# Optimization experiments

Hardware: AMD Instinct MI355X
Metric: run time of the kernel (lower is better)

Reference implementation:

```python
import jax, jax.numpy as jnp
import numpy as np

B, T, D, H = 2, 2048, 512, 8
HD = D // H  # head_dim = 64


def setup_inputs() -> dict:
    key = jax.random.key(0)
    k1, k2, k3, k4 = jax.random.split(key, 4)
    scale = 1.0 / np.sqrt(D)
    x = jax.random.normal(k1, (B, T, D), dtype=jnp.float32)
    periods = jax.random.randint(k2, (B, H), 0, 64, dtype=jnp.int32)
    w_qkv = jax.random.normal(k3, (3 * D, D), dtype=jnp.float32) * scale
    b_qkv = jnp.zeros((3 * D,), dtype=jnp.float32)
    w_out = jax.random.normal(k4, (D, D), dtype=jnp.float32) * scale
    b_out = jnp.zeros((D,), dtype=jnp.float32)
    return {"x": x, "periods": periods, "w_qkv": w_qkv, "b_qkv": b_qkv,
            "w_out": w_out, "b_out": b_out}


def reference(x, periods, w_qkv, b_qkv, w_out, b_out):
    # qkv projection: (B,T,3D) -> (3,B,H,T,HD)
    qkv = x @ w_qkv.T + b_qkv
    qkv = qkv.reshape(B, T, 3, H, HD).transpose(2, 0, 3, 1, 4)
    q, k, v = qkv[0], qkv[1], qkv[2]

    # periodic-causal mask: valid iff j <= i and (i-j) % p == 0, p = max(period,1)
    i_idx = jnp.arange(T, dtype=jnp.int32)[:, None]   # (T,1)
    j_idx = jnp.arange(T, dtype=jnp.int32)[None, :]   # (1,T)
    diff = i_idx - j_idx                              # (T,T)
    p = jnp.maximum(periods, 1)[:, :, None, None]     # (B,H,1,1)
    valid = (diff >= 0) & ((diff % p) == 0)           # (B,H,T,T)

    scores = jnp.einsum('bhqd,bhkd->bhqk', q, k) / np.sqrt(HD)
    scores = jnp.where(valid, scores, jnp.finfo(scores.dtype).min)
    attn = jax.nn.softmax(scores, axis=-1)

    out = jnp.einsum('bhqk,bhkd->bhqd', attn, v)
    out = out.transpose(0, 2, 1, 3).reshape(B, T, D)
    return out @ w_out.T + b_out
```

## Files before the change

kernel.cpp:

```cpp
#include <hip/hip_runtime.h>
#include <math.h>

#define B_  2
#define T_  2048
#define D_  512
#define H_  8
#define HD_ 64
#define QKVS (3*D_)

typedef __bf16 bf16x8 __attribute__((ext_vector_type(8)));
typedef float  f32x4  __attribute__((ext_vector_type(4)));

__device__ inline unsigned short f2bf(float f) {
  unsigned int u = __float_as_uint(f);
  return (unsigned short)((u + 0x7FFFu + ((u >> 16) & 1u)) >> 16);
}
__device__ inline unsigned int pack2bf(float lo, float hi) {
  return (unsigned int)f2bf(lo) | ((unsigned int)f2bf(hi) << 16);
}

__global__ void cast_all(const float* __restrict__ x,
                         const float* __restrict__ wq,
                         const float* __restrict__ wo,
                         unsigned short* __restrict__ xb,
                         unsigned short* __restrict__ wqb,
                         unsigned short* __restrict__ wob) {
  const int n_x  = (B_ * T_ * D_) / 4;
  const int n_wq = (QKVS * D_) / 4;
  const int n_wo = (D_ * D_) / 4;
  int i = blockIdx.x * blockDim.x + threadIdx.x;
  const float* src; unsigned short* dst; int off;
  if (i < n_x)                    { src = x;  dst = xb;  off = i; }
  else if (i < n_x + n_wq)        { src = wq; dst = wqb; off = i - n_x; }
  else if (i < n_x + n_wq + n_wo) { src = wo; dst = wob; off = i - n_x - n_wq; }
  else return;
  float4 v = ((const float4*)src)[off];
  ushort4 o;
  o.x = f2bf(v.x); o.y = f2bf(v.y); o.z = f2bf(v.z); o.w = f2bf(v.w);
  ((ushort4*)dst)[off] = o;
}

template<int BF16OUT>
__global__ __launch_bounds__(256, 4)
void gemm_nt_64(const unsigned short* __restrict__ A,
                const unsigned short* __restrict__ Bw,
                const float* __restrict__ bias, void* __restrict__ Cv,
                int M, int N, int K) {
  __shared__ short Asd[2][64 * 32];
  __shared__ short Bsd[2][64 * 32];

  const int tid = threadIdx.x;
  const int w   = tid >> 6;
  const int l   = tid & 63;
  const int wr  = w >> 1;
  const int wc  = w & 1;
  const int q   = l >> 4;
  const int ml  = l & 15;
  const int srow = tid >> 2;
  const int kch  = (tid & 3) * 8;

  const int rowbase = blockIdx.y * 64;
  const int colbase = blockIdx.x * 64;

  f32x4 acc[2][2] = {};

  for (int k0 = 0; k0 < K; k0 += 64) {
    __syncthreads();
    #pragma unroll
    for (int pnl = 0; pnl < 2; ++pnl) {
      const int kp = k0 + pnl * 32;
      const unsigned short* ga =
          A + (size_t)(rowbase + srow) * K + kp + kch;
      __builtin_amdgcn_global_load_lds(
          (const __attribute__((address_space(1))) void*)ga,
          (__attribute__((address_space(3))) void*)&Asd[pnl][w * 512],
          16, 0, 0);
      const unsigned short* gb =
          Bw + (size_t)(colbase + srow) * K + kp + kch;
      __builtin_amdgcn_global_load_lds(
          (const __attribute__((address_space(1))) void*)gb,
          (__attribute__((address_space(3))) void*)&Bsd[pnl][w * 512],
          16, 0, 0);
    }
    __syncthreads();

    #pragma unroll
    for (int pnl = 0; pnl < 2; ++pnl) {
      bf16x8 af[2], bfr[2];
      #pragma unroll
      for (int mi = 0; mi < 2; ++mi)
        af[mi] = *(const bf16x8*)&Asd[pnl][(wr * 32 + mi * 16 + ml) * 32 + q * 8];
      #pragma unroll
      for (int ni = 0; ni < 2; ++ni)
        bfr[ni] = *(const bf16x8*)&Bsd[pnl][(wc * 32 + ni * 16 + ml) * 32 + q * 8];
      #pragma unroll
      for (int mi = 0; mi < 2; ++mi)
        #pragma unroll
        for (int ni = 0; ni < 2; ++ni)
          acc[mi][ni] = __builtin_amdgcn_mfma_f32_16x16x32_bf16(
              af[mi], bfr[ni], acc[mi][ni], 0, 0, 0);
    }
  }

  #pragma unroll
  for (int mi = 0; mi < 2; ++mi) {
    #pragma unroll
    for (int ni = 0; ni < 2; ++ni) {
      const int col = colbase + wc * 32 + ni * 16 + ml;
      const float bv = bias[col];
      #pragma unroll
      for (int r = 0; r < 4; ++r) {
        const int row = rowbase + wr * 32 + mi * 16 + q * 4 + r;
        const float val = acc[mi][ni][r] + bv;
        if (BF16OUT)
          ((unsigned short*)Cv)[(size_t)row * N + col] = f2bf(val);
        else
          ((float*)Cv)[(size_t)row * N + col] = val;
      }
    }
  }
}

__global__ __launch_bounds__(256)
void attn_flash4(const unsigned short* __restrict__ qkv,
                 const int* __restrict__ periods,
                 unsigned short* __restrict__ ao) {
  const int bh = blockIdx.x, slot = 62 - blockIdx.y;
  int p = periods[bh]; if (p < 1) p = 1;
  const int g  = slot / p;
  const int r  = slot - g * p;
  const int L  = (T_ - 1 - r) / p + 1;
  const int q0 = g << 6;
  if (q0 >= L) return;
  const int b = bh >> 3, h = bh & 7;
  const int Lrem = L - q0;
  const int Nkb  = min(L, q0 + 64);

  const int tid  = threadIdx.x;
  const int w    = tid >> 6;
  const int lane = tid & 63;
  const int Q = lane >> 4, c = lane & 15;

  __shared__ __align__(16) unsigned short Qs[64 * 72];
  __shared__ __align__(16) unsigned short Ks[64 * 72];
  __shared__ __align__(16) unsigned short Vt[64 * 72];

  const size_t rowb = (size_t)b * T_ * QKVS + (size_t)h * HD_;

  {
    const int u = tid >> 2, ch4 = (tid & 3) * 16;
    const int t = q0 + min(u, Lrem - 1);
    const unsigned short* gq = qkv + rowb + (size_t)(r + t * p) * QKVS + ch4;
    int4 v0 = ((const int4*)gq)[0];
    int4 v1 = ((const int4*)gq)[1];
    *(int4*)&Qs[u * 72 + ch4 + 0] = v0;
    *(int4*)&Qs[u * 72 + ch4 + 8] = v1;
  }
  __syncthreads();
  bf16x8 qf[2];
  qf[0] = *(const bf16x8*)&Qs[(w * 16 + c) * 72 + Q * 8];
  qf[1] = *(const bf16x8*)&Qs[(w * 16 + c) * 72 + Q * 8 + 32];

  const int qb      = w * 16;
  const int nqw     = min(16, Lrem - qb);
  const int qglob   = q0 + qb + c;
  const int mylastk = q0 + qb + 15;

  float m_run = -3.0e38f, l_run = 0.f;
  f32x4 o[4] = {};
  const size_t kb = rowb + D_;
  const size_t vb = rowb + 2 * D_;

  const int krow = tid >> 2, koff = (tid & 3) * 16;
  const int vkey = tid & 63, vd0 = (tid >> 6) * 8;

  int4 kp0, kp1, vp0, vp1;
  {
    const int tk = min(krow, Nkb - 1);
    const int tv = min(vkey, Nkb - 1);
    const unsigned short* gk = qkv + kb + (size_t)(r + tk * p) * QKVS + koff;
    const unsigned short* gv = qkv + vb + (size_t)(r + tv * p) * QKVS;
    kp0 = ((const int4*)gk)[0];
    kp1 = ((const int4*)gk)[1];
    vp0 = *(const int4*)(gv + vd0);
    vp1 = *(const int4*)(gv + vd0 + 32);
  }

  for (int k0 = 0; k0 < Nkb; k0 += 64) {
    __syncthreads();
    {
      *(int4*)&Ks[krow * 72 + koff + 0] = kp0;
      *(int4*)&Ks[krow * 72 + koff + 8] = kp1;
      unsigned short vh0[8], vh1[8];
      *(int4*)vh0 = vp0;
      *(int4*)vh1 = vp1;
      #pragma unroll
      for (int j = 0; j < 8; ++j) {
        Vt[(vd0 + j) * 72 + vkey]      = vh0[j];
        Vt[(vd0 + 32 + j) * 72 + vkey] = vh1[j];
      }
    }
    __syncthreads();

    if (k0 + 64 < Nkb) {
      const int tk = min(k0 + 64 + krow, Nkb - 1);
      const int tv = min(k0 + 64 + vkey, Nkb - 1);
      const unsigned short* gk = qkv + kb + (size_t)(r + tk * p) * QKVS + koff;
      const unsigned short* gv = qkv + vb + (size_t)(r + tv * p) * QKVS;
      kp0 = ((const int4*)gk)[0];
      kp1 = ((const int4*)gk)[1];
      vp0 = *(const int4*)(gv + vd0);
      vp1 = *(const int4*)(gv + vd0 + 32);
    }

    if (nqw > 0 && k0 <= mylastk) {
      float pvv[16];
      float tmax = -3.0e38f;
      #pragma unroll
      for (int mt = 0; mt < 4; ++mt) {
        if (k0 + mt * 16 <= mylastk) {
          bf16x8 a0 = *(const bf16x8*)&Ks[(mt * 16 + c) * 72 + Q * 8];
          bf16x8 a1 = *(const bf16x8*)&Ks[(mt * 16 + c) * 72 + Q * 8 + 32];
          f32x4 s = {};
          s = __builtin_amdgcn_mfma_f32_16x16x32_bf16(a0, qf[0], s, 0, 0, 0);
          s = __builtin_amdgcn_mfma_f32_16x16x32_bf16(a1, qf[1], s, 0, 0, 0);
          #pragma unroll
          for (int rg = 0; rg < 4; ++rg) {
            const int kk = k0 + mt * 16 + Q * 4 + rg;
            float v = s[rg] * 0.125f;
            v = (kk <= qglob) ? v : -3.0e38f;
            pvv[mt * 4 + rg] = v;
            tmax = fmaxf(tmax, v);
          }
        } else {
          #pragma unroll
          for (int rg = 0; rg < 4; ++rg) pvv[mt * 4 + rg] = -3.0e38f;
        }
      }

      tmax = fmaxf(tmax, __shfl_xor(tmax, 16));
      tmax = fmaxf(tmax, __shfl_xor(tmax, 32));
      const float m_new = fmaxf(m_run, tmax);
      const float alpha = __expf(m_run - m_new);
      float tsum = 0.f;
      #pragma unroll
      for (int i = 0; i < 16; ++i) {
        pvv[i] = __expf(pvv[i] - m_new);
        tsum += pvv[i];
      }
      tsum += __shfl_xor(tsum, 16);
      tsum += __shfl_xor(tsum, 32);
      l_run = l_run * alpha + tsum;
      m_run = m_new;

      bf16x8 pb[2];
      const int sq2 = (Q & 1) << 1;
      #pragma unroll
      for (int kc = 0; kc < 2; ++kc) {
        unsigned int pk0[2], pk1[2];
        pk0[0] = pack2bf(pvv[kc * 8 + 0], pvv[kc * 8 + 1]);
        pk0[1] = pack2bf(pvv[kc * 8 + 2], pvv[kc * 8 + 3]);
        pk1[0] = pack2bf(pvv[kc * 8 + 4], pvv[kc * 8 + 5]);
        pk1[1] = pack2bf(pvv[kc * 8 + 6], pvv[kc * 8 + 7]);
        int dw[4];
        #pragma unroll
        for (int d = 0; d < 4; ++d) {
          const int src = ((sq2 + (d >> 1)) << 4) + c;
          const int v0 = __shfl((int)pk0[d & 1], src);
          const int v1 = __shfl((int)pk1[d & 1], src);
          dw[d] = (Q >= 2) ? v1 : v0;
        }
        int4 bi = make_int4(dw[0], dw[1], dw[2], dw[3]);
        pb[kc] = *(bf16x8*)&bi;
      }

      #pragma unroll
      for (int ch = 0; ch < 4; ++ch)
        #pragma unroll
        for (int t2 = 0; t2 < 4; ++t2) o[ch][t2] *= alpha;
      #pragma unroll
      for (int kc = 0; kc < 2; ++kc) {
        if (k0 + kc * 32 <= mylastk) {
          #pragma unroll
          for (int ch = 0; ch < 4; ++ch) {
            bf16x8 af =
                *(const bf16x8*)&Vt[(ch * 16 + c) * 72 + kc * 32 + Q * 8];
            o[ch] = __builtin_amdgcn_mfma_f32_16x16x32_bf16(af, pb[kc], o[ch],
                                                            0, 0, 0);
          }
        }
      }
    }
  }

  if (nqw > 0 && c < nqw) {
    const float invl = 1.f / l_run;
    const int tok = r + (q0 + qb + c) * p;
    unsigned int* dst =
        (unsigned int*)(ao + (size_t)(b * T_ + tok) * D_ + h * HD_);
    #pragma unroll
    for (int ch = 0; ch < 4; ++ch)
      #pragma unroll
      for (int rp = 0; rp < 2; ++rp) {
        const int dhalf = ch * 16 + Q * 4 + rp * 2;
        dst[dhalf >> 1] =
            pack2bf(o[ch][rp * 2] * invl, o[ch][rp * 2 + 1] * invl);
      }
  }
}

extern "C" void kernel_launch(void* const* d_in, const int* in_sizes, int n_in,
                              void* d_out, int out_size, void* d_ws, size_t ws_size,
                              hipStream_t stream) {
  const float* x      = (const float*)d_in[0];
  const int*   period = (const int*)  d_in[1];
  const float* w_qkv  = (const float*)d_in[2];
  const float* b_qkv  = (const float*)d_in[3];
  const float* w_out  = (const float*)d_in[4];
  const float* b_out  = (const float*)d_in[5];
  float* out = (float*)d_out;

  const int M = B_ * T_;

  char* ws = (char*)d_ws;
  unsigned short* xb   = (unsigned short*)(ws);
  unsigned short* wqb  = (unsigned short*)(ws + (size_t)M * D_ * 2);
  unsigned short* wob  = (unsigned short*)(ws + (size_t)M * D_ * 2
                                              + (size_t)QKVS * D_ * 2);
  unsigned short* qkvb = (unsigned short*)(ws + (size_t)M * D_ * 2
                                              + (size_t)QKVS * D_ * 2
                                              + (size_t)D_ * D_ * 2);
  unsigned short* aob  = xb;

  {
    const int n4 = (M * D_ + QKVS * D_ + D_ * D_) / 4;
    cast_all<<<dim3((n4 + 255) / 256), dim3(256), 0, stream>>>(
        x, w_qkv, w_out, xb, wqb, wob);
  }

  gemm_nt_64<1><<<dim3(QKVS / 64, M / 64), dim3(256), 0, stream>>>(
      xb, wqb, b_qkv, qkvb, M, QKVS, D_);

  attn_flash4<<<dim3(16, 63), dim3(256), 0, stream>>>(qkvb, period, aob);

  gemm_nt_64<0><<<dim3(D_ / 64, M / 64), dim3(256), 0, stream>>>(
      aob, wob, b_out, out, M, D_, D_);
}
```

Baseline: 107.7 us.

## Split attention over key chunks and combine partial softmax results

Adds a split-K (flash-decoding style) attention pass: each query tile's key range is divided into chunks of 512 keys launched along a third grid dimension. Each chunk writes its unnormalised output plus running max and sum to a workspace, and a new combine kernel merges them. The goal is to shorten the long serial key loops of tiles with small periods and improve load balance across the GPU. The cost is an extra kernel launch, fp32 partial-result traffic through global memory, and many early-exit blocks in the enlarged grid.

```diff
diff --git a/kernel.cpp b/kernel.cpp
--- a/kernel.cpp
+++ b/kernel.cpp
@@ -18,6 +18,9 @@
 __device__ inline unsigned int pack2bf(float lo, float hi) {
   return (unsigned int)f2bf(lo) | ((unsigned int)f2bf(hi) << 16);
 }
+
+#define PROW 68
+#define PCH  (64 * PROW)
 
 __global__ void cast_all(const float* __restrict__ x,
                          const float* __restrict__ wq,
@@ -69,14 +72,12 @@
     #pragma unroll
     for (int pnl = 0; pnl < 2; ++pnl) {
       const int kp = k0 + pnl * 32;
-      const unsigned short* ga =
-          A + (size_t)(rowbase + srow) * K + kp + kch;
+      const unsigned short* ga = A + (size_t)(rowbase + srow) * K + kp + kch;
       __builtin_amdgcn_global_load_lds(
           (const __attribute__((address_space(1))) void*)ga,
           (__attribute__((address_space(3))) void*)&Asd[pnl][w * 512],
           16, 0, 0);
-      const unsigned short* gb =
-          Bw + (size_t)(colbase + srow) * K + kp + kch;
+      const unsigned short* gb = Bw + (size_t)(colbase + srow) * K + kp + kch;
       __builtin_amdgcn_global_load_lds(
           (const __attribute__((address_space(1))) void*)gb,
           (__attribute__((address_space(3))) void*)&Bsd[pnl][w * 512],
@@ -122,9 +123,10 @@
 }
 
 __global__ __launch_bounds__(256)
-void attn_flash4(const unsigned short* __restrict__ qkv,
+void attn_flash5(const unsigned short* __restrict__ qkv,
                  const int* __restrict__ periods,
-                 unsigned short* __restrict__ ao) {
+                 unsigned short* __restrict__ ao,
+                 float* __restrict__ part) {
   const int bh = blockIdx.x, slot = 62 - blockIdx.y;
   int p = periods[bh]; if (p < 1) p = 1;
   const int g  = slot / p;
@@ -132,9 +134,15 @@
   const int L  = (T_ - 1 - r) / p + 1;
   const int q0 = g << 6;
   if (q0 >= L) return;
+  const int Nkb = min(L, q0 + 64);
+  const int nchunks = (Nkb + 511) >> 9;
+  const int chunk = blockIdx.z;
+  if (chunk >= nchunks) return;
+  const int kStart = chunk << 9;
+  const int kEnd   = min(Nkb, kStart + 512);
+
   const int b = bh >> 3, h = bh & 7;
   const int Lrem = L - q0;
-  const int Nkb  = min(L, q0 + 64);
 
   const int tid  = threadIdx.x;
   const int w    = tid >> 6;
@@ -176,8 +184,8 @@
 
   int4 kp0, kp1, vp0, vp1;
   {
-    const int tk = min(krow, Nkb - 1);
-    const int tv = min(vkey, Nkb - 1);
+    const int tk = min(kStart + krow, Nkb - 1);
+    const int tv = min(kStart + vkey, Nkb - 1);
     const unsigned short* gk = qkv + kb + (size_t)(r + tk * p) * QKVS + koff;
     const unsigned short* gv = qkv + vb + (size_t)(r + tv * p) * QKVS;
     kp0 = ((const int4*)gk)[0];
@@ -186,7 +194,7 @@
     vp1 = *(const int4*)(gv + vd0 + 32);
   }
 
-  for (int k0 = 0; k0 < Nkb; k0 += 64) {
+  for (int k0 = kStart; k0 < kEnd; k0 += 64) {
     __syncthreads();
     {
       *(int4*)&Ks[krow * 72 + koff + 0] = kp0;
@@ -202,7 +210,7 @@
     }
     __syncthreads();
 
-    if (k0 + 64 < Nkb) {
+    if (k0 + 64 < kEnd) {
       const int tk = min(k0 + 64 + krow, Nkb - 1);
       const int tv = min(k0 + 64 + vkey, Nkb - 1);
       const unsigned short* gk = qkv + kb + (size_t)(r + tk * p) * QKVS + koff;
@@ -219,7 +227,8 @@
       #pragma unroll
       for (int mt = 0; mt < 4; ++mt) {
         if (k0 + mt * 16 <= mylastk) {
-          bf16x8 a0 = *(const bf16x8*)&Ks[(mt * 16 + c) * 72 + Q * 8];
+          bf16x8 a0 = *(const bf16x8*)&Ks[((k0 - kStart + mt * 16) & 63) * 0 +
+                                          (mt * 16 + c) * 72 + Q * 8];
           bf16x8 a1 = *(const bf16x8*)&Ks[(mt * 16 + c) * 72 + Q * 8 + 32];
           f32x4 s = {};
           s = __builtin_amdgcn_mfma_f32_16x16x32_bf16(a0, qf[0], s, 0, 0, 0);
@@ -293,19 +302,78 @@
     }
   }
 
-  if (nqw > 0 && c < nqw) {
-    const float invl = 1.f / l_run;
-    const int tok = r + (q0 + qb + c) * p;
-    unsigned int* dst =
-        (unsigned int*)(ao + (size_t)(b * T_ + tok) * D_ + h * HD_);
+  if (nchunks == 1) {
+    if (nqw > 0 && c < nqw) {
+      const float invl = 1.f / l_run;
+      const int tok = r + (q0 + qb + c) * p;
+      unsigned int* dst =
+          (unsigned int*)(ao + (size_t)(b * T_ + tok) * D_ + h * HD_);
+      #pragma unroll
+      for (int ch = 0; ch < 4; ++ch)
+        #pragma unroll
+        for (int rp = 0; rp < 2; ++rp) {
+          const int dhalf = ch * 16 + Q * 4 + rp * 2;
+          dst[dhalf >> 1] =
+              pack2bf(o[ch][rp * 2] * invl, o[ch][rp * 2 + 1] * invl);
+        }
+    }
+  } else if (nqw > 0) {
+    float* row = part +
+        ((((size_t)bh * 63 + blockIdx.y) * 4 + chunk) * 64 + qb + c) * PROW;
     #pragma unroll
     for (int ch = 0; ch < 4; ++ch)
       #pragma unroll
-      for (int rp = 0; rp < 2; ++rp) {
-        const int dhalf = ch * 16 + Q * 4 + rp * 2;
-        dst[dhalf >> 1] =
-            pack2bf(o[ch][rp * 2] * invl, o[ch][rp * 2 + 1] * invl);
-      }
+      for (int t2 = 0; t2 < 4; ++t2)
+        row[ch * 16 + Q * 4 + t2] = o[ch][t2];
+    if (Q == 0) { row[64] = m_run; row[65] = l_run; }
+  }
+}
+
+__global__ __launch_bounds__(64)
+void attn_combine(const int* __restrict__ periods,
+                  const float* __restrict__ part,
+                  unsigned short* __restrict__ ao) {
+  const int bh = blockIdx.x, by = blockIdx.y, slot = 62 - by;
+  int p = periods[bh]; if (p < 1) p = 1;
+  const int g  = slot / p;
+  const int r  = slot - g * p;
+  const int L  = (T_ - 1 - r) / p + 1;
+  const int q0 = g << 6;
+  if (q0 >= L) return;
+  const int Nkb = min(L, q0 + 64);
+  const int nch = (Nkb + 511) >> 9;
+  if (nch < 2) return;
+  const int nq = min(64, L - q0);
+  const int qrow = threadIdx.x;
+  if (qrow >= nq) return;
+
+  const float* rows = part +
+      (((size_t)bh * 63 + by) * 4) * PCH + (size_t)qrow * PROW;
+
+  float mv[4], wgt[4];
+  float mstar = -3.0e38f;
+  for (int i = 0; i < nch; ++i) {
+    mv[i] = rows[i * PCH + 64];
+    mstar = fmaxf(mstar, mv[i]);
+  }
+  float wsum = 0.f;
+  for (int i = 0; i < nch; ++i) {
+    wgt[i] = __expf(mv[i] - mstar);
+    wsum += wgt[i] * rows[i * PCH + 65];
+  }
+  const float inv = 1.f / wsum;
+
+  const int b = bh >> 3, h = bh & 7;
+  const int tok = r + (q0 + qrow) * p;
+  unsigned int* dst =
+      (unsigned int*)(ao + (size_t)(b * T_ + tok) * D_ + h * HD_);
+  for (int d = 0; d < 64; d += 2) {
+    float a0 = 0.f, a1 = 0.f;
+    for (int i = 0; i < nch; ++i) {
+      a0 += wgt[i] * rows[i * PCH + d];
+      a1 += wgt[i] * rows[i * PCH + d + 1];
+    }
+    dst[d >> 1] = pack2bf(a0 * inv, a1 * inv);
   }
 }
 
@@ -330,6 +398,7 @@
   unsigned short* qkvb = (unsigned short*)(ws + (size_t)M * D_ * 2
                                               + (size_t)QKVS * D_ * 2
                                               + (size_t)D_ * D_ * 2);
+  float* part = (float*)((char*)qkvb + (size_t)M * QKVS * 2);
   unsigned short* aob  = xb;
 
   {
@@ -341,7 +410,10 @@
   gemm_nt_64<1><<<dim3(QKVS / 64, M / 64), dim3(256), 0, stream>>>(
       xb, wqb, b_qkv, qkvb, M, QKVS, D_);
 
-  attn_flash4<<<dim3(16, 63), dim3(256), 0, stream>>>(qkvb, period, aob);
+  attn_flash5<<<dim3(16, 63, 4), dim3(256), 0, stream>>>(
+      qkvb, period, aob, part);
+
+  attn_combine<<<dim3(16, 63), dim3(64), 0, stream>>>(period, part, aob);
 
   gemm_nt_64<0><<<dim3(D_ / 64, M / 64), dim3(256), 0, stream>>>(
       aob, wob, b_out, out, M, D_, D_);
```

Result: no change. 107.8 us (+0.2%).
